# Kernel optimization log

Hardware: AMD Instinct MI355X
Metric: run time of the kernel (lower is better)

## Reference

```python
import jax, jax.numpy as jnp
import numpy as np


def setup_inputs() -> dict:
    key = jax.random.key(0)
    ks = jax.random.split(key, 8)
    B, L, D, N, K = 4, 4096, 1024, 64, 4
    return {
        "x": jax.random.normal(ks[0], (B, L, D), dtype=jnp.float32),
        "conv_w": jax.random.normal(ks[1], (K, 1, D), dtype=jnp.float32) * 0.1,
        "conv_b": jnp.zeros((D,), dtype=jnp.float32),
        "Wp": jax.random.normal(ks[2], (D, 2 * N), dtype=jnp.float32) * (1.0 / np.sqrt(D)),
        "bp": jnp.zeros((2 * N,), dtype=jnp.float32),
        "Ws": jax.random.normal(ks[3], (D, N), dtype=jnp.float32) * (1.0 / np.sqrt(D)),
        "bs": jnp.zeros((N,), dtype=jnp.float32),
        "A_log": jax.random.normal(ks[4], (N,), dtype=jnp.float32) * 0.02,
        "dt_log": jax.random.normal(ks[5], (N,), dtype=jnp.float32) * 0.02,
        "Wo": jax.random.normal(ks[6], (N, D), dtype=jnp.float32) * (1.0 / np.sqrt(N)),
        "bo": jnp.zeros((D,), dtype=jnp.float32),
    }


def reference(x, conv_w, conv_b, Wp, bp, Ws, bs, A_log, dt_log, Wo, bo):
    B, L, D = x.shape
    K = conv_w.shape[0]
    N = Ws.shape[1]

    # causal depthwise conv: left-pad by K-1, sum K shifted slices (K is tiny)
    x_pad = jnp.pad(x, ((0, 0), (K - 1, 0), (0, 0)))
    conv = conv_b + sum(x_pad[:, k:k + L, :] * conv_w[k, 0] for k in range(K))

    proj = conv @ Wp + bp                     # [B, L, 2N]
    B_t = jax.nn.softplus(proj[..., :N])      # [B, L, N]
    C_t = jnp.tanh(proj[..., N:])             # [B, L, N]
    u = x @ Ws + bs                           # [B, L, N]

    A = -jax.nn.softplus(A_log)               # [N]
    dt = jax.nn.softplus(dt_log)              # [N]
    decay = 1.0 + dt * A                      # [N]

    def step(state, inputs):
        u_t, b_t, c_t = inputs                # each [B, N]
        state = decay * state + dt * b_t * u_t
        return state, c_t * state

    init = jnp.zeros((B, N), dtype=x.dtype)
    xs = tuple(jnp.swapaxes(a, 0, 1) for a in (u, B_t, C_t))  # time-major
    _, ys = jax.lax.scan(step, init, xs, unroll=4)            # [L, B, N]
    y = jnp.swapaxes(ys, 0, 1)                                # [B, L, N]
    return y @ Wo + bo                                        # [B, L, D]
```

## Files before the change

kernel.cpp:

```cpp
#include <hip/hip_runtime.h>

#define B_ 4
#define L_ 4096
#define D_ 1024
#define N_ 64

typedef _Float16 f16;
typedef __attribute__((ext_vector_type(8))) _Float16 half8;
typedef __attribute__((ext_vector_type(4))) float f32x4;

__device__ __forceinline__ float softplus_f(float x) {
    return fmaxf(x, 0.0f) + log1pf(__expf(-fabsf(x)));
}

__device__ __forceinline__ float tanh_f(float x) {
    float xc = fminf(fmaxf(x, -15.0f), 15.0f);
    float e = __expf(2.0f * xc);
    return (e - 1.0f) / (e + 1.0f);
}

__device__ __forceinline__ void bar_raw() {
    asm volatile("" ::: "memory");
    __builtin_amdgcn_s_barrier();
    asm volatile("" ::: "memory");
}

__global__ __launch_bounds__(256) void k_prepw(
    const float* __restrict__ Wp, const float* __restrict__ Ws,
    const float* __restrict__ Wo, f16* __restrict__ WT, f16* __restrict__ WoT)
{
    int gid = blockIdx.x * 256 + threadIdx.x;
    if (gid < 16384) {
        int c = gid & 127, kg = gid >> 7;
        f16 h[8];
        #pragma unroll
        for (int j = 0; j < 8; j++)
            h[j] = (f16)Wp[(size_t)(kg * 8 + j) * 128 + c];
        *(uint4*)&WT[(size_t)c * 1024 + kg * 8] = *(uint4*)h;
    } else if (gid < 24576) {
        int idx = gid - 16384;
        int c = idx & 63, kg = idx >> 6;
        f16 h[8];
        #pragma unroll
        for (int j = 0; j < 8; j++)
            h[j] = (f16)Ws[(size_t)(kg * 8 + j) * 64 + c];
        *(uint4*)&WT[(size_t)(128 + c) * 1024 + kg * 8] = *(uint4*)h;
    } else {
        int idx = gid - 24576;
        int d = idx & 1023, ng = idx >> 10;
        f16 h[8];
        #pragma unroll
        for (int j = 0; j < 8; j++)
            h[j] = (f16)Wo[(size_t)(ng * 8 + j) * D_ + d];
        *(uint4*)&WoT[(size_t)d * 64 + ng * 8] = *(uint4*)h;
    }
}

__global__ __launch_bounds__(512, 2) void k_frontend(
    const float* __restrict__ x, const float* __restrict__ conv_w,
    const float* __restrict__ conv_b, const f16* __restrict__ WT,
    const float* __restrict__ bp, const float* __restrict__ bs,
    const float* __restrict__ dt_log,
    f16* __restrict__ zT, f16* __restrict__ cT)
{
    __shared__ __align__(16) char smem[65536];
    char* wt0 = smem;
    char* wt1 = smem + 24576;
    char* chb = smem + 49152;
    char* xhb = smem + 57344;
    float* sE = (float*)smem;

    const int tid = threadIdx.x;
    const int w = tid >> 6, lane = tid & 63;
    const int r = lane & 15, q = lane >> 4;
    const int wr = w >> 2, wc = w & 3;
    const int T0 = blockIdx.x * 64;
    const int bb = T0 >> 12, l0 = T0 & (L_ - 1);
    const int cbase = wc * 48;
    const int ct0 = (tid >> 4) * 2;
    const int cd  = (tid & 15) * 4;

    f32x4 acc[3][2] = {};

    #define WLOAD(RS, c) { _Pragma("unroll") \
        for (int s = 0; s < 3; s++) { \
            int slot = tid + 512 * s; \
            RS[s] = *(const uint4*)&WT[(size_t)(slot >> 3) * 1024 + (c) * 64 + (slot & 7) * 8]; \
        } }
    #define DSWT(BUF, RS) { _Pragma("unroll") \
        for (int s = 0; s < 3; s++) { \
            int slot = tid + 512 * s; int row = slot >> 3, g = slot & 7; \
            *(uint4*)((BUF) + row * 128 + ((g * 16) ^ ((row & 7) << 4))) = RS[s]; \
        } }
    #define XWLOAD(RX, RW, c) { _Pragma("unroll") \
        for (int i = 0; i < 5; i++) { \
            int l = l0 + ct0 - 3 + i; \
            f32x4 v = {0.f, 0.f, 0.f, 0.f}; \
            if (l >= 0) v = *(const f32x4*)&x[((size_t)(bb * L_ + l)) * D_ + (c) * 64 + cd]; \
            RX[i] = v; } \
        _Pragma("unroll") \
        for (int k = 0; k < 4; k++) \
            RW[k] = *(const f32x4*)&conv_w[k * D_ + (c) * 64 + cd]; \
        RW[4] = *(const f32x4*)&conv_b[(c) * 64 + cd]; }

    #define CONV(RX, RW) { _Pragma("unroll") \
        for (int tt = 0; tt < 2; tt++) { \
            const int t = ct0 + tt; \
            f16 hc4[4], hx4[4]; \
            _Pragma("unroll") \
            for (int j = 0; j < 4; j++) { \
                float s0 = RW[4][j]; \
                s0 = fmaf(RW[0][j], RX[tt + 0][j], s0); \
                s0 = fmaf(RW[1][j], RX[tt + 1][j], s0); \
                s0 = fmaf(RW[2][j], RX[tt + 2][j], s0); \
                s0 = fmaf(RW[3][j], RX[tt + 3][j], s0); \
                hc4[j] = (f16)s0; hx4[j] = (f16)RX[tt + 3][j]; \
            } \
            const int cb = (cd * 2) ^ ((t & 7) << 4); \
            *(uint2*)(chb + t * 128 + cb) = *(uint2*)hc4; \
            *(uint2*)(xhb + t * 128 + cb) = *(uint2*)hx4; \
        } }

    #define MFMA_PH(WTC) { \
        const bool nC = (cbase < 128); \
        const bool nX = (cbase + 32 >= 128); \
        _Pragma("unroll") \
        for (int ks = 0; ks < 2; ks++) { \
            const int cb16 = ks * 64 + q * 16; \
            half8 a8[3]; \
            _Pragma("unroll") \
            for (int mf = 0; mf < 3; mf++) { \
                const int ar = cbase + mf * 16 + r; \
                a8[mf] = *(const half8*)((WTC) + ar * 128 + (cb16 ^ ((ar & 7) << 4))); \
            } \
            _Pragma("unroll") \
            for (int nf = 0; nf < 2; nf++) { \
                const int tr = wr * 32 + nf * 16 + r; \
                const int tb = cb16 ^ ((tr & 7) << 4); \
                half8 bc = {}, bx = {}; \
                if (nC) bc = *(const half8*)(chb + tr * 128 + tb); \
                if (nX) bx = *(const half8*)(xhb + tr * 128 + tb); \
                acc[0][nf] = __builtin_amdgcn_mfma_f32_16x16x32_f16( \
                    a8[0], (cbase < 128) ? bc : bx, acc[0][nf], 0, 0, 0); \
                acc[1][nf] = __builtin_amdgcn_mfma_f32_16x16x32_f16( \
                    a8[1], (cbase + 16 < 128) ? bc : bx, acc[1][nf], 0, 0, 0); \
                acc[2][nf] = __builtin_amdgcn_mfma_f32_16x16x32_f16( \
                    a8[2], (cbase + 32 < 128) ? bc : bx, acc[2][nf], 0, 0, 0); \
            } \
        } }

    #define CHUNK(c, RX, RW, RSN, RXN, RWN, WTC, WTN, PF) { \
        if (PF) { WLOAD(RSN, (c) + 1); XWLOAD(RXN, RWN, (c) + 1); } \
        CONV(RX, RW); \
        asm volatile("s_waitcnt lgkmcnt(0)" ::: "memory"); \
        __builtin_amdgcn_sched_barrier(0); \
        __builtin_amdgcn_s_barrier(); \
        asm volatile("" ::: "memory"); \
        MFMA_PH(WTC); \
        if (PF) { DSWT(WTN, RSN); } \
        bar_raw(); }

    f32x4 rXa[5], rWa[5], rXb[5], rWb[5];
    uint4 rSa[3], rSb[3];

    WLOAD(rSa, 0);
    XWLOAD(rXa, rWa, 0);
    DSWT(wt0, rSa);
    __syncthreads();

    #pragma unroll 1
    for (int cc = 0; cc < 8; cc++) {
        const int c0 = cc * 2;
        CHUNK(c0,     rXa, rWa, rSb, rXb, rWb, wt0, wt1, true);
        CHUNK(c0 + 1, rXb, rWb, rSa, rXa, rWa, wt1, wt0, (c0 + 1) < 15);
    }

    float* sB = sE;
    float* sC = sE + 64 * 68;
    float* sU = sE + 2 * 64 * 68;
    #pragma unroll
    for (int mf = 0; mf < 3; mf++) {
        const int cb4 = cbase + mf * 16 + q * 4;
        const int seg = cb4 >> 6;
        const int cl = cb4 & 63;
        const float4 bb4 = (seg == 2) ? *(const float4*)&bs[cl]
                                      : *(const float4*)&bp[cb4];
        float* dst = (seg == 0) ? sB : (seg == 1 ? sC : sU);
        #pragma unroll
        for (int nf = 0; nf < 2; nf++) {
            const int t = wr * 32 + nf * 16 + r;
            float v0 = acc[mf][nf][0] + bb4.x;
            float v1 = acc[mf][nf][1] + bb4.y;
            float v2 = acc[mf][nf][2] + bb4.z;
            float v3 = acc[mf][nf][3] + bb4.w;
            if (seg == 0) {
                v0 = softplus_f(v0); v1 = softplus_f(v1);
                v2 = softplus_f(v2); v3 = softplus_f(v3);
            } else if (seg == 1) {
                v0 = tanh_f(v0); v1 = tanh_f(v1);
                v2 = tanh_f(v2); v3 = tanh_f(v3);
            }
            float4 vv = {v0, v1, v2, v3};
            *(float4*)&dst[t * 68 + cl] = vv;
        }
    }
    __syncthreads();

    {
        const int n = tid >> 3, tg = tid & 7;
        const float dtv = softplus_f(dt_log[n]);
        f16 hz[8], hc2[8];
        #pragma unroll
        for (int j = 0; j < 8; j++) {
            const int t = tg * 8 + j;
            hz[j] = (f16)(dtv * sB[t * 68 + n] * sU[t * 68 + n]);
            hc2[j] = (f16)sC[t * 68 + n];
        }
        size_t o = ((size_t)(bb * N_ + n)) * L_ + l0 + tg * 8;
        *(uint4*)&zT[o] = *(uint4*)hz;
        *(uint4*)&cT[o] = *(uint4*)hc2;
    }
    #undef WLOAD
    #undef DSWT
    #undef XWLOAD
    #undef CONV
    #undef MFMA_PH
    #undef CHUNK
}

#define ZI(i) ((i) + ((i) >> 4))
__global__ __launch_bounds__(256) void k_scan(
    const f16* __restrict__ zT, const f16* __restrict__ cT,
    const float* __restrict__ A_log, const float* __restrict__ dt_log,
    f16* __restrict__ yH)
{
    __shared__ float zs[4352];
    __shared__ float cs[4352];
    __shared__ float sA[4], sB[4];
    const int bn = blockIdx.x;
    const int n = bn & (N_ - 1);
    const int tid = threadIdx.x;
    const int lane = tid & 63, w = tid >> 6;
    const f16* zp = zT + (size_t)bn * L_;
    const f16* cp = cT + (size_t)bn * L_;

    #pragma unroll
    for (int it = 0; it < 2; it++) {
        int i = tid * 8 + it * 2048;
        uint4 rz = *(const uint4*)(zp + i);
        uint4 rc = *(const uint4*)(cp + i);
        const f16* hz = (const f16*)&rz;
        const f16* hc = (const f16*)&rc;
        #pragma unroll
        for (int k = 0; k < 8; k++) {
            zs[ZI(i + k)] = (float)hz[k];
            cs[ZI(i + k)] = (float)hc[k];
        }
    }
    __syncthreads();

    float dtv = softplus_f(dt_log[n]);
    float Av = -softplus_f(A_log[n]);
    float dec = fmaf(dtv, Av, 1.0f);

    const int base = tid * 17;
    float s = 0.0f;
    #pragma unroll
    for (int j = 0; j < 16; j++) s = fmaf(dec, s, zs[base + j]);

    float d2 = dec * dec, d4 = d2 * d2, d8 = d4 * d4, d16 = d8 * d8;

    float Ag = d16, Bg = s;
    #pragma unroll
    for (int off = 1; off < 64; off <<= 1) {
        float Ap = __shfl_up(Ag, off);
        float Bp = __shfl_up(Bg, off);
        if (lane >= off) { Bg = fmaf(Ag, Bp, Bg); Ag *= Ap; }
    }
    if (lane == 63) { sA[w] = Ag; sB[w] = Bg; }
    __syncthreads();

    float Bc = 0.0f;
    for (int i = 0; i < w; i++) Bc = fmaf(sA[i], Bc, sB[i]);
    float Ae = __shfl_up(Ag, 1);
    float Be = __shfl_up(Bg, 1);
    if (lane == 0) { Ae = 1.0f; Be = 0.0f; }
    float carry = fmaf(Ae, Bc, Be);

    float st = carry;
    #pragma unroll
    for (int j = 0; j < 16; j++) {
        st = fmaf(dec, st, zs[base + j]);
        zs[base + j] = cs[base + j] * st;
    }
    __syncthreads();

    f16* yp = yH + (size_t)bn * L_;
    #pragma unroll
    for (int it = 0; it < 2; it++) {
        int i = tid * 8 + it * 2048;
        f16 h[8];
        #pragma unroll
        for (int k = 0; k < 8; k++) h[k] = (f16)zs[ZI(i + k)];
        *(uint4*)&yp[i] = *(uint4*)h;
    }
}
#undef ZI

__global__ __launch_bounds__(256) void k_out(
    const f16* __restrict__ yH, const f16* __restrict__ WoT,
    const float* __restrict__ bo, float* __restrict__ out)
{
    __shared__ __align__(16) f16 ys[64 * 72];
    const int tid = threadIdx.x;
    const int w = tid >> 6, lane = tid & 63;
    const int r = lane & 15, q = lane >> 4;
    const int T0 = blockIdx.x * 64;
    const int bb = T0 >> 12, l0 = T0 & (L_ - 1);
    const int dw = blockIdx.y * 128 + w * 32;

    {
        const int n = tid & 63, tg = tid >> 6;
        #pragma unroll
        for (int h2 = 0; h2 < 2; h2++) {
            uint4 v = *(const uint4*)&yH[((size_t)(bb * N_ + n)) * L_ + l0 + tg * 16 + h2 * 8];
            const f16* hh = (const f16*)&v;
            #pragma unroll
            for (int j = 0; j < 8; j++)
                ys[(tg * 16 + h2 * 8 + j) * 72 + n] = hh[j];
        }
    }
    __syncthreads();

    f32x4 acc[2][4] = {};
    #pragma unroll
    for (int ks = 0; ks < 2; ks++) {
        const int kk = ks * 32 + q * 8;
        half8 af[2];
        #pragma unroll
        for (int mf = 0; mf < 2; mf++)
            af[mf] = *(const half8*)&WoT[(size_t)(dw + mf * 16 + r) * 64 + kk];
        #pragma unroll
        for (int nf = 0; nf < 4; nf++) {
            half8 bf = *(const half8*)&ys[(nf * 16 + r) * 72 + kk];
            #pragma unroll
            for (int mf = 0; mf < 2; mf++)
                acc[mf][nf] = __builtin_amdgcn_mfma_f32_16x16x32_f16(
                    af[mf], bf, acc[mf][nf], 0, 0, 0);
        }
    }

    #pragma unroll
    for (int mf = 0; mf < 2; mf++) {
        const int d = dw + mf * 16 + q * 4;
        const float4 bb4 = *(const float4*)&bo[d];
        #pragma unroll
        for (int nf = 0; nf < 4; nf++) {
            const int t = T0 + nf * 16 + r;
            float4 o = {acc[mf][nf][0] + bb4.x, acc[mf][nf][1] + bb4.y,
                        acc[mf][nf][2] + bb4.z, acc[mf][nf][3] + bb4.w};
            *(float4*)&out[(size_t)t * D_ + d] = o;
        }
    }
}

extern "C" void kernel_launch(void* const* d_in, const int* in_sizes, int n_in,
                              void* d_out, int out_size, void* d_ws, size_t ws_size,
                              hipStream_t stream) {
    const float* x      = (const float*)d_in[0];
    const float* conv_w = (const float*)d_in[1];
    const float* conv_b = (const float*)d_in[2];
    const float* Wp     = (const float*)d_in[3];
    const float* bp     = (const float*)d_in[4];
    const float* Ws     = (const float*)d_in[5];
    const float* bs     = (const float*)d_in[6];
    const float* A_log  = (const float*)d_in[7];
    const float* dt_log = (const float*)d_in[8];
    const float* Wo     = (const float*)d_in[9];
    const float* bo     = (const float*)d_in[10];
    float* out = (float*)d_out;

    char* wsp = (char*)d_ws;
    f16* WT  = (f16*)wsp;
    f16* WoT = (f16*)(wsp + 393216);
    f16* zT  = (f16*)(wsp + 524288);
    f16* cT  = (f16*)(wsp + 2621440);
    f16* yH  = (f16*)(wsp + 4718592);

    k_prepw<<<dim3(128), dim3(256), 0, stream>>>(Wp, Ws, Wo, WT, WoT);
    k_frontend<<<dim3(B_ * L_ / 64), dim3(512), 0, stream>>>(
        x, conv_w, conv_b, WT, bp, bs, dt_log, zT, cT);
    k_scan<<<dim3(B_ * N_), dim3(256), 0, stream>>>(zT, cT, A_log, dt_log, yH);
    k_out<<<dim3(B_ * L_ / 64, D_ / 128), dim3(256), 0, stream>>>(yH, WoT, bo, out);
}
```

Measured before the change: 188.0 us.

## Shrink frontend tile to 32 timesteps, stage conv weights in LDS, pad rows

The frontend kernel now processes 32 timesteps per block instead of 64. It doubles the grid and raises the launch-bounds occupancy target from 2 to 4 blocks, while each wave computes one N-fragment instead of two. Conv weights and bias are copied once into shared memory rather than reloaded from global memory per chunk. The XOR-swizzled LDS layout is replaced by a padded row stride of 136 bytes to avoid bank conflicts. In exchange, each block reloads the full projection weight matrix for half as much work, which doubles weight traffic across the grid, and the 81 KB of shared memory per block may limit how many blocks actually fit.

```diff
diff --git a/kernel.cpp b/kernel.cpp
--- a/kernel.cpp
+++ b/kernel.cpp
@@ -56,31 +56,35 @@
     }
 }
 
-__global__ __launch_bounds__(512, 2) void k_frontend(
+#define WST 136
+__global__ __launch_bounds__(512, 4) void k_frontend(
     const float* __restrict__ x, const float* __restrict__ conv_w,
     const float* __restrict__ conv_b, const f16* __restrict__ WT,
     const float* __restrict__ bp, const float* __restrict__ bs,
     const float* __restrict__ dt_log,
     f16* __restrict__ zT, f16* __restrict__ cT)
 {
-    __shared__ __align__(16) char smem[65536];
+    __shared__ __align__(16) char smem[81408];
     char* wt0 = smem;
-    char* wt1 = smem + 24576;
-    char* chb = smem + 49152;
-    char* xhb = smem + 57344;
-    float* sE = (float*)smem;
+    char* wt1 = smem + 26112;
+    char* chb = smem + 52224;
+    char* xhb = smem + 56576;
+    float* cwS = (float*)(smem + 60928);
+    float* sE  = (float*)smem;
 
     const int tid = threadIdx.x;
     const int w = tid >> 6, lane = tid & 63;
     const int r = lane & 15, q = lane >> 4;
-    const int wr = w >> 2, wc = w & 3;
-    const int T0 = blockIdx.x * 64;
+    const int wc = w & 3, wn = w >> 2;
+    const int T0 = blockIdx.x * 32;
     const int bb = T0 >> 12, l0 = T0 & (L_ - 1);
     const int cbase = wc * 48;
-    const int ct0 = (tid >> 4) * 2;
-    const int cd  = (tid & 15) * 4;
-
-    f32x4 acc[3][2] = {};
+    const int ct = tid >> 4;
+    const int cd = (tid & 15) * 4;
+
+    f32x4 acc[3] = {};
+    f32x4 rXa[4], rXb[4];
+    uint4 rSa[3], rSb[3];
 
     #define WLOAD(RS, c) { _Pragma("unroll") \
         for (int s = 0; s < 3; s++) { \
@@ -89,69 +93,59 @@
         } }
     #define DSWT(BUF, RS) { _Pragma("unroll") \
         for (int s = 0; s < 3; s++) { \
-            int slot = tid + 512 * s; int row = slot >> 3, g = slot & 7; \
-            *(uint4*)((BUF) + row * 128 + ((g * 16) ^ ((row & 7) << 4))) = RS[s]; \
+            int slot = tid + 512 * s; \
+            *(uint4*)((BUF) + (slot >> 3) * WST + (slot & 7) * 16) = RS[s]; \
         } }
-    #define XWLOAD(RX, RW, c) { _Pragma("unroll") \
-        for (int i = 0; i < 5; i++) { \
-            int l = l0 + ct0 - 3 + i; \
+    #define XLOAD(RX, c) { _Pragma("unroll") \
+        for (int i = 0; i < 4; i++) { \
+            int l = l0 + ct - 3 + i; \
             f32x4 v = {0.f, 0.f, 0.f, 0.f}; \
             if (l >= 0) v = *(const f32x4*)&x[((size_t)(bb * L_ + l)) * D_ + (c) * 64 + cd]; \
-            RX[i] = v; } \
+            RX[i] = v; } }
+    #define CONV(RX, c) { \
+        const int dg = (c) * 64 + cd; \
+        f32x4 w0 = *(const f32x4*)&cwS[dg]; \
+        f32x4 w1 = *(const f32x4*)&cwS[1024 + dg]; \
+        f32x4 w2 = *(const f32x4*)&cwS[2048 + dg]; \
+        f32x4 w3 = *(const f32x4*)&cwS[3072 + dg]; \
+        f32x4 cb = *(const f32x4*)&cwS[4096 + dg]; \
+        f16 hc4[4], hx4[4]; \
         _Pragma("unroll") \
-        for (int k = 0; k < 4; k++) \
-            RW[k] = *(const f32x4*)&conv_w[k * D_ + (c) * 64 + cd]; \
-        RW[4] = *(const f32x4*)&conv_b[(c) * 64 + cd]; }
-
-    #define CONV(RX, RW) { _Pragma("unroll") \
-        for (int tt = 0; tt < 2; tt++) { \
-            const int t = ct0 + tt; \
-            f16 hc4[4], hx4[4]; \
-            _Pragma("unroll") \
-            for (int j = 0; j < 4; j++) { \
-                float s0 = RW[4][j]; \
-                s0 = fmaf(RW[0][j], RX[tt + 0][j], s0); \
-                s0 = fmaf(RW[1][j], RX[tt + 1][j], s0); \
-                s0 = fmaf(RW[2][j], RX[tt + 2][j], s0); \
-                s0 = fmaf(RW[3][j], RX[tt + 3][j], s0); \
-                hc4[j] = (f16)s0; hx4[j] = (f16)RX[tt + 3][j]; \
-            } \
-            const int cb = (cd * 2) ^ ((t & 7) << 4); \
-            *(uint2*)(chb + t * 128 + cb) = *(uint2*)hc4; \
-            *(uint2*)(xhb + t * 128 + cb) = *(uint2*)hx4; \
-        } }
+        for (int j = 0; j < 4; j++) { \
+            float s0 = cb[j]; \
+            s0 = fmaf(w0[j], RX[0][j], s0); \
+            s0 = fmaf(w1[j], RX[1][j], s0); \
+            s0 = fmaf(w2[j], RX[2][j], s0); \
+            s0 = fmaf(w3[j], RX[3][j], s0); \
+            hc4[j] = (f16)s0; hx4[j] = (f16)RX[3][j]; \
+        } \
+        *(uint2*)(chb + ct * WST + cd * 2) = *(uint2*)hc4; \
+        *(uint2*)(xhb + ct * WST + cd * 2) = *(uint2*)hx4; }
 
     #define MFMA_PH(WTC) { \
         const bool nC = (cbase < 128); \
         const bool nX = (cbase + 32 >= 128); \
         _Pragma("unroll") \
         for (int ks = 0; ks < 2; ks++) { \
-            const int cb16 = ks * 64 + q * 16; \
-            half8 a8[3]; \
-            _Pragma("unroll") \
-            for (int mf = 0; mf < 3; mf++) { \
-                const int ar = cbase + mf * 16 + r; \
-                a8[mf] = *(const half8*)((WTC) + ar * 128 + (cb16 ^ ((ar & 7) << 4))); \
-            } \
-            _Pragma("unroll") \
-            for (int nf = 0; nf < 2; nf++) { \
-                const int tr = wr * 32 + nf * 16 + r; \
-                const int tb = cb16 ^ ((tr & 7) << 4); \
-                half8 bc = {}, bx = {}; \
-                if (nC) bc = *(const half8*)(chb + tr * 128 + tb); \
-                if (nX) bx = *(const half8*)(xhb + tr * 128 + tb); \
-                acc[0][nf] = __builtin_amdgcn_mfma_f32_16x16x32_f16( \
-                    a8[0], (cbase < 128) ? bc : bx, acc[0][nf], 0, 0, 0); \
-                acc[1][nf] = __builtin_amdgcn_mfma_f32_16x16x32_f16( \
-                    a8[1], (cbase + 16 < 128) ? bc : bx, acc[1][nf], 0, 0, 0); \
-                acc[2][nf] = __builtin_amdgcn_mfma_f32_16x16x32_f16( \
-                    a8[2], (cbase + 32 < 128) ? bc : bx, acc[2][nf], 0, 0, 0); \
-            } \
+            const int cbyte = ks * 64 + q * 16; \
+            const int tr = wn * 16 + r; \
+            half8 a0 = *(const half8*)((WTC) + (cbase +      r) * WST + cbyte); \
+            half8 a1 = *(const half8*)((WTC) + (cbase + 16 + r) * WST + cbyte); \
+            half8 a2 = *(const half8*)((WTC) + (cbase + 32 + r) * WST + cbyte); \
+            half8 bc = {}, bx = {}; \
+            if (nC) bc = *(const half8*)(chb + tr * WST + cbyte); \
+            if (nX) bx = *(const half8*)(xhb + tr * WST + cbyte); \
+            acc[0] = __builtin_amdgcn_mfma_f32_16x16x32_f16( \
+                a0, (cbase < 128) ? bc : bx, acc[0], 0, 0, 0); \
+            acc[1] = __builtin_amdgcn_mfma_f32_16x16x32_f16( \
+                a1, (cbase + 16 < 128) ? bc : bx, acc[1], 0, 0, 0); \
+            acc[2] = __builtin_amdgcn_mfma_f32_16x16x32_f16( \
+                a2, (cbase + 32 < 128) ? bc : bx, acc[2], 0, 0, 0); \
         } }
 
-    #define CHUNK(c, RX, RW, RSN, RXN, RWN, WTC, WTN, PF) { \
-        if (PF) { WLOAD(RSN, (c) + 1); XWLOAD(RXN, RWN, (c) + 1); } \
-        CONV(RX, RW); \
+    #define CHUNK(c, RXc, RSN, RXN, WTC, WTN, PF) { \
+        if (PF) { WLOAD(RSN, (c) + 1); XLOAD(RXN, (c) + 1); } \
+        CONV(RXc, c); \
         asm volatile("s_waitcnt lgkmcnt(0)" ::: "memory"); \
         __builtin_amdgcn_sched_barrier(0); \
         __builtin_amdgcn_s_barrier(); \
@@ -160,24 +154,31 @@
         if (PF) { DSWT(WTN, RSN); } \
         bar_raw(); }
 
-    f32x4 rXa[5], rWa[5], rXb[5], rWb[5];
-    uint4 rSa[3], rSb[3];
+    #pragma unroll
+    for (int i = 0; i < 3; i++) {
+        int idx = tid + 512 * i;
+        if (idx < 1280) {
+            float4 v = (idx < 1024) ? ((const float4*)conv_w)[idx]
+                                    : ((const float4*)conv_b)[idx - 1024];
+            ((float4*)cwS)[idx] = v;
+        }
+    }
 
     WLOAD(rSa, 0);
-    XWLOAD(rXa, rWa, 0);
+    XLOAD(rXa, 0);
     DSWT(wt0, rSa);
     __syncthreads();
 
     #pragma unroll 1
     for (int cc = 0; cc < 8; cc++) {
         const int c0 = cc * 2;
-        CHUNK(c0,     rXa, rWa, rSb, rXb, rWb, wt0, wt1, true);
-        CHUNK(c0 + 1, rXb, rWb, rSa, rXa, rWa, wt1, wt0, (c0 + 1) < 15);
+        CHUNK(c0,     rXa, rSb, rXb, wt0, wt1, true);
+        CHUNK(c0 + 1, rXb, rSa, rXa, wt1, wt0, (c0 + 1) < 15);
     }
 
     float* sB = sE;
-    float* sC = sE + 64 * 68;
-    float* sU = sE + 2 * 64 * 68;
+    float* sC = sE + 32 * 68;
+    float* sU = sE + 2 * 32 * 68;
     #pragma unroll
     for (int mf = 0; mf < 3; mf++) {
         const int cb4 = cbase + mf * 16 + q * 4;
@@ -186,47 +187,45 @@
         const float4 bb4 = (seg == 2) ? *(const float4*)&bs[cl]
                                       : *(const float4*)&bp[cb4];
         float* dst = (seg == 0) ? sB : (seg == 1 ? sC : sU);
-        #pragma unroll
-        for (int nf = 0; nf < 2; nf++) {
-            const int t = wr * 32 + nf * 16 + r;
-            float v0 = acc[mf][nf][0] + bb4.x;
-            float v1 = acc[mf][nf][1] + bb4.y;
-            float v2 = acc[mf][nf][2] + bb4.z;
-            float v3 = acc[mf][nf][3] + bb4.w;
-            if (seg == 0) {
-                v0 = softplus_f(v0); v1 = softplus_f(v1);
-                v2 = softplus_f(v2); v3 = softplus_f(v3);
-            } else if (seg == 1) {
-                v0 = tanh_f(v0); v1 = tanh_f(v1);
-                v2 = tanh_f(v2); v3 = tanh_f(v3);
-            }
-            float4 vv = {v0, v1, v2, v3};
-            *(float4*)&dst[t * 68 + cl] = vv;
-        }
+        const int t = wn * 16 + r;
+        float v0 = acc[mf][0] + bb4.x;
+        float v1 = acc[mf][1] + bb4.y;
+        float v2 = acc[mf][2] + bb4.z;
+        float v3 = acc[mf][3] + bb4.w;
+        if (seg == 0) {
+            v0 = softplus_f(v0); v1 = softplus_f(v1);
+            v2 = softplus_f(v2); v3 = softplus_f(v3);
+        } else if (seg == 1) {
+            v0 = tanh_f(v0); v1 = tanh_f(v1);
+            v2 = tanh_f(v2); v3 = tanh_f(v3);
+        }
+        float4 vv = {v0, v1, v2, v3};
+        *(float4*)&dst[t * 68 + cl] = vv;
     }
     __syncthreads();
 
     {
         const int n = tid >> 3, tg = tid & 7;
         const float dtv = softplus_f(dt_log[n]);
-        f16 hz[8], hc2[8];
-        #pragma unroll
-        for (int j = 0; j < 8; j++) {
-            const int t = tg * 8 + j;
+        f16 hz[4], hc2[4];
+        #pragma unroll
+        for (int j = 0; j < 4; j++) {
+            const int t = tg * 4 + j;
             hz[j] = (f16)(dtv * sB[t * 68 + n] * sU[t * 68 + n]);
             hc2[j] = (f16)sC[t * 68 + n];
         }
-        size_t o = ((size_t)(bb * N_ + n)) * L_ + l0 + tg * 8;
-        *(uint4*)&zT[o] = *(uint4*)hz;
-        *(uint4*)&cT[o] = *(uint4*)hc2;
+        size_t o = ((size_t)(bb * N_ + n)) * L_ + l0 + tg * 4;
+        *(uint2*)&zT[o] = *(uint2*)hz;
+        *(uint2*)&cT[o] = *(uint2*)hc2;
     }
     #undef WLOAD
     #undef DSWT
-    #undef XWLOAD
+    #undef XLOAD
     #undef CONV
     #undef MFMA_PH
     #undef CHUNK
 }
+#undef WST
 
 #define ZI(i) ((i) + ((i) >> 4))
 __global__ __launch_bounds__(256) void k_scan(
@@ -388,7 +387,7 @@
     f16* yH  = (f16*)(wsp + 4718592);
 
     k_prepw<<<dim3(128), dim3(256), 0, stream>>>(Wp, Ws, Wo, WT, WoT);
-    k_frontend<<<dim3(B_ * L_ / 64), dim3(512), 0, stream>>>(
+    k_frontend<<<dim3(B_ * L_ / 32), dim3(512), 0, stream>>>(
         x, conv_w, conv_b, WT, bp, bs, dt_log, zT, cT);
     k_scan<<<dim3(B_ * N_), dim3(256), 0, stream>>>(zT, cT, A_log, dt_log, yH);
     k_out<<<dim3(B_ * L_ / 64, D_ / 128), dim3(256), 0, stream>>>(yH, WoT, bo, out);
```

After: 238.6 us. 26.9% more time.
